# Kernel optimization log

Measured on AMD Instinct MI355X. Metric: run time of the kernel, lower is better.

The kernel has to match this reference:

```python
import jax, jax.numpy as jnp
import numpy as np

N_NODES = 50000
N_EDGES = 800000
D_FEAT = 128
HIDDEN = 128
OUT = 64
HEADS = 4


def setup_inputs() -> dict:
    key = jax.random.key(0)
    ks = jax.random.split(key, 12)
    s_in = 1.0 / np.sqrt(D_FEAT)
    s_h = 1.0 / np.sqrt(HIDDEN)
    x = jax.random.normal(ks[0], (N_NODES, D_FEAT), dtype=jnp.float32)
    edge_index = jax.random.randint(ks[1], (2, N_EDGES), 0, N_NODES, dtype=jnp.int32)
    return {
        "x": x,
        "edge_index": edge_index,
        # SAGEConv params: lin_l (aggregated neighbors), lin_r (root), bias
        "W_l": jax.random.normal(ks[2], (D_FEAT, HIDDEN), dtype=jnp.float32) * s_in,
        "W_r": jax.random.normal(ks[3], (D_FEAT, HIDDEN), dtype=jnp.float32) * s_in,
        "b_sage": jnp.zeros((HIDDEN,), dtype=jnp.float32),
        # GATConv params: lin_src, lin_dst (heads*hidden each), att vectors, bias
        "W_src": jax.random.normal(ks[4], (HIDDEN, HEADS * HIDDEN), dtype=jnp.float32) * s_h,
        "W_dst": jax.random.normal(ks[5], (HIDDEN, HEADS * HIDDEN), dtype=jnp.float32) * s_h,
        "att_src": jax.random.normal(ks[6], (HEADS, HIDDEN), dtype=jnp.float32) * s_h,
        "att_dst": jax.random.normal(ks[7], (HEADS, HIDDEN), dtype=jnp.float32) * s_h,
        "b_gat": jnp.zeros((HIDDEN,), dtype=jnp.float32),
        # Final Linear
        "W_lin": jax.random.normal(ks[8], (HIDDEN, OUT), dtype=jnp.float32) * s_h,
        "b_lin": jnp.zeros((OUT,), dtype=jnp.float32),
    }


def reference(x, edge_index, W_l, W_r, b_sage, W_src, W_dst, att_src, att_dst, b_gat, W_lin, b_lin):
    N = x.shape[0]
    src = edge_index[0]
    dst = edge_index[1]

    # ---- SAGEConv (mean aggregation): out = lin_l(mean_j x_j) + lin_r(x_i) + b ----
    agg = jax.ops.segment_sum(x[src], dst, num_segments=N)          # [N, d]
    cnt = jax.ops.segment_sum(jnp.ones_like(dst, dtype=x.dtype), dst, num_segments=N)
    mean_nbr = agg / jnp.maximum(cnt, 1.0)[:, None]
    h = mean_nbr @ W_l + x @ W_r + b_sage                           # [N, H*... no: [N, hidden]
    h = jax.nn.relu(h)

    # ---- GATConv (heads=4, concat=False -> mean over heads) ----
    H, C = att_src.shape
    hs = (h @ W_src).reshape(N, H, C)                               # source-transformed [N, H, C]
    hd = (h @ W_dst).reshape(N, H, C)                               # dest-transformed   [N, H, C]
    a_s = jnp.einsum('nhc,hc->nh', hs, att_src)                     # [N, H]
    a_d = jnp.einsum('nhc,hc->nh', hd, att_dst)                     # [N, H]
    e = jax.nn.leaky_relu(a_s[src] + a_d[dst], negative_slope=0.2)  # [E, H]
    # edge softmax over incoming edges per destination node
    e_max = jax.ops.segment_max(e, dst, num_segments=N)             # [N, H]
    e_exp = jnp.exp(e - e_max[dst])                                 # [E, H]
    denom = jax.ops.segment_sum(e_exp, dst, num_segments=N)         # [N, H]
    alpha = e_exp / denom[dst]                                      # [E, H]
    msg = hs[src] * alpha[:, :, None]                               # [E, H, C]
    out = jax.ops.segment_sum(msg, dst, num_segments=N)             # [N, H, C]
    out = out.mean(axis=1) + b_gat                                  # concat=False: avg heads
    out = jax.nn.relu(out)

    # ---- final Linear ----
    return out @ W_lin + b_lin
```

## Files before the change

### kernel.cpp

```cpp
#include <hip/hip_runtime.h>

#define D 128
#define HEADS 4

typedef __attribute__((ext_vector_type(8))) short short8;
typedef __attribute__((ext_vector_type(4))) float f32x4;

static __device__ __forceinline__ float leaky(float v) { return v > 0.f ? v : 0.2f * v; }

static __device__ __forceinline__ float2 bf2_to_f2(unsigned int u) {
    float2 r;
    union { unsigned int i; float f; } a, b;
    a.i = (u & 0xffffu) << 16;
    b.i = u & 0xffff0000u;
    r.x = a.f; r.y = b.f;
    return r;
}
static __device__ __forceinline__ float bf_to_f(unsigned short s) {
    union { unsigned int i; float f; } a;
    a.i = ((unsigned int)s) << 16;
    return a.f;
}
static __device__ __forceinline__ unsigned short f2bf(float f) {
    union { float f; unsigned int i; } v; v.f = f;
    unsigned int u = v.i;
    unsigned int r = (u + 0x7fffu + ((u >> 16) & 1u)) >> 16;
    return (unsigned short)r;
}

#define CPAD 16
#define PREP_CNT 107520
#define MAXBUCK 2048
#define BSLOT 1024
#define CH 8192

__global__ __launch_bounds__(256) void k_early(const float* __restrict__ x, int npairs,
                                               const float* __restrict__ Wl, const float* __restrict__ Wr,
                                               const float* __restrict__ Wsrc, const float* __restrict__ Wlin,
                                               const float* __restrict__ Wdst,
                                               const float* __restrict__ atts, const float* __restrict__ attd,
                                               unsigned short* __restrict__ Bh,
                                               unsigned short* __restrict__ Bg,
                                               unsigned short* __restrict__ Bf,
                                               float* __restrict__ wsd,
                                               unsigned int* __restrict__ xb) {
    int i = blockIdx.x * 256 + threadIdx.x;
    if (i < 32768) {
        int idx = i;
        int j = idx & 7, n16 = (idx >> 3) & 15, quad = (idx >> 7) & 3, rest = idx >> 9;
        int nc = rest & 7, kb = rest >> 3;
        int kk = kb * 32 + quad * 8 + j;
        int n = nc * 16 + n16;
        float v = (kk < 128) ? Wl[kk * 128 + n] : Wr[(kk - 128) * 128 + n];
        Bh[idx] = f2bf(v);
    } else if (i < 32768 + 65536) {
        int idx = i - 32768;
        int j = idx & 7, n16 = (idx >> 3) & 15, quad = (idx >> 7) & 3, rest = idx >> 9;
        int nc = rest & 7, kb = rest >> 3;
        int kk = kb * 32 + quad * 8 + j;
        int n = nc * 16 + n16;
        float v = Wsrc[(kk & 127) * 512 + (kk >> 7) * 128 + n];
        Bg[idx] = f2bf(v);
    } else if (i < 32768 + 65536 + 8192) {
        int idx = i - 98304;
        int j = idx & 7, n16 = (idx >> 3) & 15, quad = (idx >> 7) & 3, rest = idx >> 9;
        int nc = rest & 3, kb = rest >> 2;
        int kk = kb * 32 + quad * 8 + j;
        int n = nc * 16 + n16;
        Bf[idx] = f2bf(Wlin[kk * 64 + n]);
    } else if (i < PREP_CNT) {
        int tt = i - 106496;
        int k = tt >> 3, o = tt & 7;
        int hh = o & 3;
        const float* W = (o < 4) ? Wsrc : Wdst;
        const float* att = (o < 4) ? atts : attd;
        float acc = 0.f;
        for (int c = 0; c < 128; c++) acc += W[k * 512 + hh * 128 + c] * att[hh * 128 + c];
        wsd[k * 8 + o] = acc;
    } else {
        int p = i - PREP_CNT;
        if (p < npairs) {
            float2 v = *(const float2*)(x + (size_t)p * 2);
            xb[p] = (unsigned int)f2bf(v.x) | ((unsigned int)f2bf(v.y) << 16);
        }
    }
}

__global__ __launch_bounds__(256) void k_scatter1(const int* __restrict__ ei, int E, int nbuck,
                                                  int* __restrict__ bcur,
                                                  unsigned int* __restrict__ ebuf) {
    __shared__ unsigned int sval[CH];
    __shared__ unsigned short soff[CH];
    __shared__ int cnt[MAXBUCK];
    __shared__ int gbase[MAXBUCK];
    int t = threadIdx.x;
    int c0 = blockIdx.x * CH;
    int ecnt = E - c0; if (ecnt > CH) ecnt = CH;
    for (int i = t; i < MAXBUCK; i += 256) cnt[i] = 0;
    __syncthreads();
    for (int i = t; i < ecnt; i += 256) {
        int s = ei[c0 + i], d = ei[E + c0 + i];
        int b = d >> 5;
        soff[i] = (unsigned short)atomicAdd(&cnt[b], 1);
        sval[i] = (unsigned int)s | ((unsigned int)(d & 31) << 16) | ((unsigned int)b << 21);
    }
    __syncthreads();
    for (int b = t; b < nbuck; b += 256)
        if (cnt[b]) gbase[b] = (b << 10) + atomicAdd(&bcur[b * CPAD], cnt[b]);
    __syncthreads();
    for (int i = t; i < ecnt; i += 256) {
        unsigned int v = sval[i];
        int b = v >> 21;
        int pos = gbase[b] + soff[i];
        if (pos < ((b + 1) << 10)) ebuf[pos] = v & 0x1fffffu;
    }
}

#define BCAP 1024
__global__ __launch_bounds__(256) void k_build_sage(const unsigned int* __restrict__ ebuf,
                                                    const int* __restrict__ bcur,
                                                    const unsigned int* __restrict__ xb,
                                                    int* __restrict__ csr,
                                                    int* __restrict__ rowptr,
                                                    int* __restrict__ rowend,
                                                    unsigned int* __restrict__ meanb, int N) {
    __shared__ int cnt[32];
    __shared__ int excl[33];
    __shared__ unsigned char off[BCAP];
    __shared__ unsigned int rawv[BCAP];
    __shared__ int sorted[BCAP];
    int b = blockIdx.x, t = threadIdx.x;
    int e0 = b << 10;
    int ecnt = bcur[b * CPAD];
    if (ecnt > BCAP) ecnt = BCAP;
    if (t < 32) cnt[t] = 0;
    __syncthreads();
    for (int i = t; i < ecnt; i += 256) {
        unsigned int p = ebuf[e0 + i];
        rawv[i] = p;
        off[i] = (unsigned char)atomicAdd(&cnt[(p >> 16) & 31], 1);
    }
    __syncthreads();
    if (t == 0) {
        int run = 0;
        #pragma unroll
        for (int j = 0; j < 32; j++) { excl[j] = run; run += cnt[j]; }
        excl[32] = run;
    }
    __syncthreads();
    for (int i = t; i < ecnt; i += 256) {
        unsigned int p = rawv[i];
        int d = (p >> 16) & 31;
        sorted[excl[d] + off[i]] = (int)(p & 0xffffu);
    }
    __syncthreads();
    int nb0 = b << 5;
    if (t < 32 && nb0 + t < N) {
        rowptr[nb0 + t] = e0 + excl[t];
        rowend[nb0 + t] = e0 + excl[t + 1];
    }
    for (int i = t; i < ecnt; i += 256) csr[e0 + i] = sorted[i];
    int wv = t >> 6, lane = t & 63;
    for (int k = 0; k < 8; k++) {
        int local = wv * 8 + k;
        int node = nb0 + local;
        if (node >= N) continue;
        int le0 = excl[local], le1 = excl[local + 1];
        float ax = 0.f, ay = 0.f;
        int e = le0;
        for (; e + 3 < le1; e += 4) {
            int s0 = sorted[e], s1 = sorted[e + 1], s2 = sorted[e + 2], s3 = sorted[e + 3];
            unsigned int u0 = xb[(size_t)s0 * 64 + lane];
            unsigned int u1 = xb[(size_t)s1 * 64 + lane];
            unsigned int u2 = xb[(size_t)s2 * 64 + lane];
            unsigned int u3 = xb[(size_t)s3 * 64 + lane];
            float2 v0 = bf2_to_f2(u0), v1 = bf2_to_f2(u1), v2 = bf2_to_f2(u2), v3 = bf2_to_f2(u3);
            ax += (v0.x + v1.x) + (v2.x + v3.x);
            ay += (v0.y + v1.y) + (v2.y + v3.y);
        }
        for (; e < le1; e++) {
            float2 v0 = bf2_to_f2(xb[(size_t)sorted[e] * 64 + lane]);
            ax += v0.x; ay += v0.y;
        }
        int dg = le1 - le0;
        float inv = 1.0f / (float)(dg > 0 ? dg : 1);
        unsigned int o = (unsigned int)f2bf(ax * inv) | ((unsigned int)f2bf(ay * inv) << 16);
        __builtin_nontemporal_store(o, meanb + (size_t)node * 64 + lane);
    }
}

__global__ __launch_bounds__(256) void k_mfma_h(const unsigned short* __restrict__ A0,
                                                const unsigned short* __restrict__ A1,
                                                const unsigned short* __restrict__ Bp,
                                                const float* __restrict__ bias,
                                                const float* __restrict__ wsd,
                                                unsigned short* __restrict__ outb,
                                                float* __restrict__ a_s,
                                                float* __restrict__ a_d, int M) {
    const int NC = 8;
    __shared__ unsigned short sH[64][136];
    __shared__ float swsd[1024];
    int tid = threadIdx.x;
    int wave = tid >> 6;
    int lane = tid & 63;
    int row0 = blockIdx.x * 64 + wave * 16;
    int n16 = lane & 15, quad = lane >> 4;
    int arow = row0 + n16;
    int arowc = arow < M ? arow : 0;
    for (int i = tid; i < 1024; i += 256) swsd[i] = wsd[i];
    f32x4 acc[NC];
    #pragma unroll
    for (int i = 0; i < NC; i++) acc[i] = (f32x4){0.f, 0.f, 0.f, 0.f};
    #pragma unroll
    for (int kb = 0; kb < 8; kb++) {
        const unsigned short* ap = (kb < 4)
            ? (A0 + (size_t)arowc * 128 + kb * 32 + quad * 8)
            : (A1 + (size_t)arowc * 128 + (kb - 4) * 32 + quad * 8);
        short8 af = *(const short8*)ap;
        #pragma unroll
        for (int nc = 0; nc < NC; nc++) {
            short8 bf = *(const short8*)(Bp + ((((size_t)(kb * NC + nc) * 4 + quad) * 16 + n16) << 3));
            acc[nc] = __builtin_amdgcn_mfma_f32_16x16x32_bf16(af, bf, acc[nc], 0, 0, 0);
        }
    }
    int orow = row0 + quad * 4;
    int lrow = wave * 16 + quad * 4;
    #pragma unroll
    for (int r = 0; r < 4; r++) {
        int m = orow + r;
        #pragma unroll
        for (int nc = 0; nc < NC; nc++) {
            int col = nc * 16 + n16;
            float v = fmaxf(acc[nc][r] + bias[col], 0.f);
            unsigned short bv = f2bf(v);
            sH[lrow + r][col] = bv;
            if (m < M) outb[(size_t)m * 128 + col] = bv;
        }
    }
    __syncthreads();
    #pragma unroll
    for (int j = tid; j < 512; j += 256) {
        int m = j >> 3, o = j & 7;
        float accd = 0.f;
        #pragma unroll 4
        for (int k = 0; k < 128; k++)
            accd += bf_to_f(sH[m][k]) * swsd[k * 8 + o];
        int n = blockIdx.x * 64 + m;
        if (n < M) {
            if (o < 4) a_s[n * 4 + o] = accd;
            else       a_d[n * 4 + (o - 4)] = accd;
        }
    }
}

#define EDGE_CAP 192
__global__ __launch_bounds__(256) void k_gat_agg(const int* __restrict__ rowptr,
                                                 const int* __restrict__ rowend,
                                                 const int* __restrict__ csr,
                                                 const unsigned int* __restrict__ hb,
                                                 const float* __restrict__ a_s,
                                                 const float* __restrict__ a_d,
                                                 unsigned int* __restrict__ aggb, int N) {
    __shared__ int   sOff[4][EDGE_CAP];
    __shared__ float sAl[4][EDGE_CAP * 4];
    int wv = threadIdx.x >> 6;
    int lane = threadIdx.x & 63;
    int n = blockIdx.x * 4 + wv;
    bool active = n < N;
    int e0 = 0, deg = 0;
    float4 ad = {0.f, 0.f, 0.f, 0.f};
    if (active) {
        e0 = rowptr[n];
        deg = rowend[n] - e0;
        ad = *(const float4*)(a_d + (size_t)n * 4);
    }
    f32x4 psum = {0.f, 0.f, 0.f, 0.f};
    for (int base = 0; base < deg; base += 64) {
        int i = base + lane;
        if (i < deg) {
            int s = csr[e0 + i];
            float4 as = *(const float4*)(a_s + (size_t)s * 4);
            f32x4 w;
            w.x = __expf(leaky(as.x + ad.x));
            w.y = __expf(leaky(as.y + ad.y));
            w.z = __expf(leaky(as.z + ad.z));
            w.w = __expf(leaky(as.w + ad.w));
            psum += w;
            if (i < EDGE_CAP) {
                sOff[wv][i] = s << 8;
                *(f32x4*)&sAl[wv][i * 4] = w;
            }
        }
    }
    #pragma unroll
    for (int o = 32; o; o >>= 1) {
        psum.x += __shfl_xor(psum.x, o);
        psum.y += __shfl_xor(psum.y, o);
        psum.z += __shfl_xor(psum.z, o);
        psum.w += __shfl_xor(psum.w, o);
    }
    f32x4 inv;
    inv.x = psum.x > 0.f ? 0.25f / psum.x : 0.f;
    inv.y = psum.y > 0.f ? 0.25f / psum.y : 0.f;
    inv.z = psum.z > 0.f ? 0.25f / psum.z : 0.f;
    inv.w = psum.w > 0.f ? 0.25f / psum.w : 0.f;
    int capdeg = deg < EDGE_CAP ? deg : EDGE_CAP;
    for (int base = 0; base < capdeg; base += 64) {
        int i = base + lane;
        if (i < capdeg) {
            f32x4 w = *(f32x4*)&sAl[wv][i * 4];
            w *= inv;
            *(f32x4*)&sAl[wv][i * 4] = w;
        }
    }
    const char* hbL = (const char*)hb + lane * 4;
    float2 ac0 = {0, 0}, ac1 = {0, 0}, ac2 = {0, 0}, ac3 = {0, 0};
    int e = 0;
    for (; e + 7 < capdeg; e += 8) {
        unsigned int u[8];
        #pragma unroll
        for (int q = 0; q < 8; q++)
            u[q] = *(const unsigned int*)(hbL + sOff[wv][e + q]);
        #pragma unroll
        for (int q = 0; q < 8; q++) {
            f32x4 w = *(const f32x4*)&sAl[wv][(e + q) * 4];
            float2 v = bf2_to_f2(u[q]);
            ac0.x += w.x * v.x; ac0.y += w.x * v.y;
            ac1.x += w.y * v.x; ac1.y += w.y * v.y;
            ac2.x += w.z * v.x; ac2.y += w.z * v.y;
            ac3.x += w.w * v.x; ac3.y += w.w * v.y;
        }
    }
    for (; e + 3 < capdeg; e += 4) {
        unsigned int u[4];
        #pragma unroll
        for (int q = 0; q < 4; q++)
            u[q] = *(const unsigned int*)(hbL + sOff[wv][e + q]);
        #pragma unroll
        for (int q = 0; q < 4; q++) {
            f32x4 w = *(const f32x4*)&sAl[wv][(e + q) * 4];
            float2 v = bf2_to_f2(u[q]);
            ac0.x += w.x * v.x; ac0.y += w.x * v.y;
            ac1.x += w.y * v.x; ac1.y += w.y * v.y;
            ac2.x += w.z * v.x; ac2.y += w.z * v.y;
            ac3.x += w.w * v.x; ac3.y += w.w * v.y;
        }
    }
    for (; e < capdeg; e++) {
        unsigned int u0 = *(const unsigned int*)(hbL + sOff[wv][e]);
        f32x4 w0 = *(const f32x4*)&sAl[wv][e * 4];
        float2 v0 = bf2_to_f2(u0);
        ac0.x += w0.x * v0.x; ac0.y += w0.x * v0.y;
        ac1.x += w0.y * v0.x; ac1.y += w0.y * v0.y;
        ac2.x += w0.z * v0.x; ac2.y += w0.z * v0.y;
        ac3.x += w0.w * v0.x; ac3.y += w0.w * v0.y;
    }
    for (int i = EDGE_CAP; i < deg; i++) {
        int s = csr[e0 + i];
        float4 as = *(const float4*)(a_s + (size_t)s * 4);
        f32x4 w;
        w.x = __expf(leaky(as.x + ad.x)) * inv.x;
        w.y = __expf(leaky(as.y + ad.y)) * inv.y;
        w.z = __expf(leaky(as.z + ad.z)) * inv.z;
        w.w = __expf(leaky(as.w + ad.w)) * inv.w;
        float2 v0 = bf2_to_f2(hb[(size_t)s * 64 + lane]);
        ac0.x += w.x * v0.x; ac0.y += w.x * v0.y;
        ac1.x += w.y * v0.x; ac1.y += w.y * v0.y;
        ac2.x += w.z * v0.x; ac2.y += w.z * v0.y;
        ac3.x += w.w * v0.x; ac3.y += w.w * v0.y;
    }
    if (!active) return;
    unsigned int* rowu = aggb + (size_t)n * 256 + lane;
    unsigned int o0 = (unsigned int)f2bf(ac0.x) | ((unsigned int)f2bf(ac0.y) << 16);
    unsigned int o1 = (unsigned int)f2bf(ac1.x) | ((unsigned int)f2bf(ac1.y) << 16);
    unsigned int o2 = (unsigned int)f2bf(ac2.x) | ((unsigned int)f2bf(ac2.y) << 16);
    unsigned int o3 = (unsigned int)f2bf(ac3.x) | ((unsigned int)f2bf(ac3.y) << 16);
    __builtin_nontemporal_store(o0, rowu + 0);
    __builtin_nontemporal_store(o1, rowu + 64);
    __builtin_nontemporal_store(o2, rowu + 128);
    __builtin_nontemporal_store(o3, rowu + 192);
}

__global__ __launch_bounds__(256) void k_mfma_tail(const unsigned short* __restrict__ aggb,
                                                   const unsigned short* __restrict__ Bg,
                                                   const float* __restrict__ bg,
                                                   const unsigned short* __restrict__ Bf,
                                                   const float* __restrict__ bl,
                                                   float* __restrict__ out, int M) {
    __shared__ unsigned short sG[64][136];
    int wave = threadIdx.x >> 6;
    int lane = threadIdx.x & 63;
    int row0 = blockIdx.x * 64 + wave * 16;
    int n16 = lane & 15, quad = lane >> 4;
    {
        int arow = row0 + n16;
        int arowc = arow < M ? arow : 0;
        const unsigned short* ap = aggb + (size_t)arowc * 512 + quad * 8;
        f32x4 acc[8];
        #pragma unroll
        for (int i = 0; i < 8; i++) acc[i] = (f32x4){0.f, 0.f, 0.f, 0.f};
        #pragma unroll
        for (int kb = 0; kb < 16; kb++) {
            short8 af = *(const short8*)(ap + kb * 32);
            #pragma unroll
            for (int nc = 0; nc < 8; nc++) {
                short8 bf = *(const short8*)(Bg + ((((size_t)(kb * 8 + nc) * 4 + quad) * 16 + n16) << 3));
                acc[nc] = __builtin_amdgcn_mfma_f32_16x16x32_bf16(af, bf, acc[nc], 0, 0, 0);
            }
        }
        int lrow = wave * 16 + quad * 4;
        #pragma unroll
        for (int r = 0; r < 4; r++) {
            #pragma unroll
            for (int nc = 0; nc < 8; nc++) {
                int col = nc * 16 + n16;
                sG[lrow + r][col] = f2bf(fmaxf(acc[nc][r] + bg[col], 0.f));
            }
        }
    }
    __syncthreads();
    {
        f32x4 acc[4];
        #pragma unroll
        for (int i = 0; i < 4; i++) acc[i] = (f32x4){0.f, 0.f, 0.f, 0.f};
        #pragma unroll
        for (int kb = 0; kb < 4; kb++) {
            short8 af = *(const short8*)&sG[wave * 16 + n16][kb * 32 + quad * 8];
            #pragma unroll
            for (int nc = 0; nc < 4; nc++) {
                short8 bf = *(const short8*)(Bf + ((((size_t)(kb * 4 + nc) * 4 + quad) * 16 + n16) << 3));
                acc[nc] = __builtin_amdgcn_mfma_f32_16x16x32_bf16(af, bf, acc[nc], 0, 0, 0);
            }
        }
        int orow = row0 + quad * 4;
        #pragma unroll
        for (int r = 0; r < 4; r++) {
            int m = orow + r;
            if (m < M) {
                #pragma unroll
                for (int nc = 0; nc < 4; nc++) {
                    int col = nc * 16 + n16;
                    out[(size_t)m * 64 + col] = acc[nc][r] + bl[col];
                }
            }
        }
    }
}

extern "C" void kernel_launch(void* const* d_in, const int* in_sizes, int n_in,
                              void* d_out, int out_size, void* d_ws, size_t ws_size,
                              hipStream_t stream) {
    const float* x    = (const float*)d_in[0];
    const int*   ei   = (const int*)d_in[1];
    const float* Wl   = (const float*)d_in[2];
    const float* Wr   = (const float*)d_in[3];
    const float* bs   = (const float*)d_in[4];
    const float* Wsrc = (const float*)d_in[5];
    const float* Wdst = (const float*)d_in[6];
    const float* atts = (const float*)d_in[7];
    const float* attd = (const float*)d_in[8];
    const float* bg   = (const float*)d_in[9];
    const float* Wlin = (const float*)d_in[10];
    const float* bl   = (const float*)d_in[11];
    int N = in_sizes[0] / D;
    int E = in_sizes[1] / 2;
    int nbuck = (N + 31) >> 5;
    int npairs = N * 64;

    char* w = (char*)d_ws;
    auto alloc = [&](size_t bytes) {
        char* p = w;
        w += (bytes + 255) & ~(size_t)255;
        return p;
    };
    unsigned int* xb     = (unsigned int*)alloc((size_t)N * 256);
    unsigned int* meanb  = (unsigned int*)alloc((size_t)N * 256);
    unsigned int* hb     = (unsigned int*)alloc((size_t)N * 256);
    unsigned int* aggb   = (unsigned int*)alloc((size_t)N * 1024);
    unsigned short* Bh   = (unsigned short*)alloc(65536 * 2);
    unsigned short* Bg   = (unsigned short*)alloc(65536 * 2);
    unsigned short* Bf   = (unsigned short*)alloc(8192 * 2);
    float* a_s           = (float*)alloc((size_t)N * 16);
    float* a_d           = (float*)alloc((size_t)N * 16);
    float* wsd           = (float*)alloc(1024 * 4);
    int* rowptr          = (int*)alloc((size_t)N * 4);
    int* rowend          = (int*)alloc((size_t)N * 4);
    int* bcur            = (int*)alloc((size_t)MAXBUCK * CPAD * 4);
    unsigned int* ebuf   = (unsigned int*)alloc((size_t)MAXBUCK * BSLOT * 4);
    int* csr             = (int*)alloc((size_t)MAXBUCK * BSLOT * 4);
    (void)ws_size; (void)n_in; (void)out_size;

    hipMemsetAsync(bcur, 0, (size_t)MAXBUCK * CPAD * 4, stream);

    int workBlocks = (PREP_CNT + npairs + 255) / 256;
    k_early<<<workBlocks, 256, 0, stream>>>(x, npairs, Wl, Wr, Wsrc, Wlin, Wdst, atts, attd,
                                            Bh, Bg, Bf, wsd, xb);
    k_scatter1<<<(E + CH - 1) / CH, 256, 0, stream>>>(ei, E, nbuck, bcur, ebuf);
    k_build_sage<<<nbuck, 256, 0, stream>>>(ebuf, bcur, xb, csr, rowptr, rowend, meanb, N);

    k_mfma_h<<<(N + 63) / 64, 256, 0, stream>>>((const unsigned short*)meanb,
                                                (const unsigned short*)xb, Bh, bs, wsd,
                                                (unsigned short*)hb, a_s, a_d, N);
    k_gat_agg<<<(N + 3) / 4, 256, 0, stream>>>(rowptr, rowend, csr, hb, a_s, a_d, aggb, N);
    k_mfma_tail<<<(N + 63) / 64, 256, 0, stream>>>((const unsigned short*)aggb, Bg, bg,
                                                   Bf, bl, (float*)d_out, N);
}
```

Measured before the change: 260.0 us.

## Fuse edge scatter into prep kernel and simplify GAT aggregation loop

Merges the bucket scatter kernel into the early prep kernel by dispatching the first blocks to scatter work, removing one launch. The GAT aggregation inner loop now stores source indices instead of byte offsets, uses a single 4-way unrolled loop with tree-summed FMAs, and adds a block barrier. The fused kernel allocates the scatter's large shared-memory arrays for every block, which may reduce occupancy of the elementwise prep blocks, and the smaller unroll lowers memory-level parallelism in the gather.

```diff
diff --git a/kernel.cpp b/kernel.cpp
--- a/kernel.cpp
+++ b/kernel.cpp
@@ -35,6 +35,9 @@
 #define CH 8192
 
 __global__ __launch_bounds__(256) void k_early(const float* __restrict__ x, int npairs,
+                                               const int* __restrict__ ei, int E, int nbuck, int scatB,
+                                               int* __restrict__ bcur,
+                                               unsigned int* __restrict__ ebuf,
                                                const float* __restrict__ Wl, const float* __restrict__ Wr,
                                                const float* __restrict__ Wsrc, const float* __restrict__ Wlin,
                                                const float* __restrict__ Wdst,
@@ -44,7 +47,35 @@
                                                unsigned short* __restrict__ Bf,
                                                float* __restrict__ wsd,
                                                unsigned int* __restrict__ xb) {
-    int i = blockIdx.x * 256 + threadIdx.x;
+    __shared__ unsigned int sval[CH];
+    __shared__ unsigned short soff[CH];
+    __shared__ int cnt[MAXBUCK];
+    __shared__ int gbase[MAXBUCK];
+    int gb = blockIdx.x, t = threadIdx.x;
+    if (gb < scatB) {
+        int c0 = gb * CH;
+        int ecnt = E - c0; if (ecnt > CH) ecnt = CH;
+        for (int i = t; i < MAXBUCK; i += 256) cnt[i] = 0;
+        __syncthreads();
+        for (int i = t; i < ecnt; i += 256) {
+            int s = ei[c0 + i], d = ei[E + c0 + i];
+            int b = d >> 5;
+            soff[i] = (unsigned short)atomicAdd(&cnt[b], 1);
+            sval[i] = (unsigned int)s | ((unsigned int)(d & 31) << 16) | ((unsigned int)b << 21);
+        }
+        __syncthreads();
+        for (int b = t; b < nbuck; b += 256)
+            if (cnt[b]) gbase[b] = (b << 10) + atomicAdd(&bcur[b * CPAD], cnt[b]);
+        __syncthreads();
+        for (int i = t; i < ecnt; i += 256) {
+            unsigned int v = sval[i];
+            int b = v >> 21;
+            int pos = gbase[b] + soff[i];
+            if (pos < ((b + 1) << 10)) ebuf[pos] = v & 0x1fffffu;
+        }
+        return;
+    }
+    int i = (gb - scatB) * 256 + t;
     if (i < 32768) {
         int idx = i;
         int j = idx & 7, n16 = (idx >> 3) & 15, quad = (idx >> 7) & 3, rest = idx >> 9;
@@ -86,36 +117,6 @@
     }
 }
 
-__global__ __launch_bounds__(256) void k_scatter1(const int* __restrict__ ei, int E, int nbuck,
-                                                  int* __restrict__ bcur,
-                                                  unsigned int* __restrict__ ebuf) {
-    __shared__ unsigned int sval[CH];
-    __shared__ unsigned short soff[CH];
-    __shared__ int cnt[MAXBUCK];
-    __shared__ int gbase[MAXBUCK];
-    int t = threadIdx.x;
-    int c0 = blockIdx.x * CH;
-    int ecnt = E - c0; if (ecnt > CH) ecnt = CH;
-    for (int i = t; i < MAXBUCK; i += 256) cnt[i] = 0;
-    __syncthreads();
-    for (int i = t; i < ecnt; i += 256) {
-        int s = ei[c0 + i], d = ei[E + c0 + i];
-        int b = d >> 5;
-        soff[i] = (unsigned short)atomicAdd(&cnt[b], 1);
-        sval[i] = (unsigned int)s | ((unsigned int)(d & 31) << 16) | ((unsigned int)b << 21);
-    }
-    __syncthreads();
-    for (int b = t; b < nbuck; b += 256)
-        if (cnt[b]) gbase[b] = (b << 10) + atomicAdd(&bcur[b * CPAD], cnt[b]);
-    __syncthreads();
-    for (int i = t; i < ecnt; i += 256) {
-        unsigned int v = sval[i];
-        int b = v >> 21;
-        int pos = gbase[b] + soff[i];
-        if (pos < ((b + 1) << 10)) ebuf[pos] = v & 0x1fffffu;
-    }
-}
-
 #define BCAP 1024
 __global__ __launch_bounds__(256) void k_build_sage(const unsigned int* __restrict__ ebuf,
                                                     const int* __restrict__ bcur,
@@ -261,7 +262,7 @@
                                                  const float* __restrict__ a_s,
                                                  const float* __restrict__ a_d,
                                                  unsigned int* __restrict__ aggb, int N) {
-    __shared__ int   sOff[4][EDGE_CAP];
+    __shared__ int   sSrc[4][EDGE_CAP];
     __shared__ float sAl[4][EDGE_CAP * 4];
     int wv = threadIdx.x >> 6;
     int lane = threadIdx.x & 63;
@@ -287,7 +288,7 @@
             w.w = __expf(leaky(as.w + ad.w));
             psum += w;
             if (i < EDGE_CAP) {
-                sOff[wv][i] = s << 8;
+                sSrc[wv][i] = s;
                 *(f32x4*)&sAl[wv][i * 4] = w;
             }
         }
@@ -313,42 +314,33 @@
             *(f32x4*)&sAl[wv][i * 4] = w;
         }
     }
-    const char* hbL = (const char*)hb + lane * 4;
+    __syncthreads();
     float2 ac0 = {0, 0}, ac1 = {0, 0}, ac2 = {0, 0}, ac3 = {0, 0};
     int e = 0;
-    for (; e + 7 < capdeg; e += 8) {
-        unsigned int u[8];
-        #pragma unroll
-        for (int q = 0; q < 8; q++)
-            u[q] = *(const unsigned int*)(hbL + sOff[wv][e + q]);
-        #pragma unroll
-        for (int q = 0; q < 8; q++) {
-            f32x4 w = *(const f32x4*)&sAl[wv][(e + q) * 4];
-            float2 v = bf2_to_f2(u[q]);
-            ac0.x += w.x * v.x; ac0.y += w.x * v.y;
-            ac1.x += w.y * v.x; ac1.y += w.y * v.y;
-            ac2.x += w.z * v.x; ac2.y += w.z * v.y;
-            ac3.x += w.w * v.x; ac3.y += w.w * v.y;
-        }
-    }
     for (; e + 3 < capdeg; e += 4) {
-        unsigned int u[4];
-        #pragma unroll
-        for (int q = 0; q < 4; q++)
-            u[q] = *(const unsigned int*)(hbL + sOff[wv][e + q]);
-        #pragma unroll
-        for (int q = 0; q < 4; q++) {
-            f32x4 w = *(const f32x4*)&sAl[wv][(e + q) * 4];
-            float2 v = bf2_to_f2(u[q]);
-            ac0.x += w.x * v.x; ac0.y += w.x * v.y;
-            ac1.x += w.y * v.x; ac1.y += w.y * v.y;
-            ac2.x += w.z * v.x; ac2.y += w.z * v.y;
-            ac3.x += w.w * v.x; ac3.y += w.w * v.y;
-        }
+        int s0 = sSrc[wv][e], s1 = sSrc[wv][e + 1], s2 = sSrc[wv][e + 2], s3 = sSrc[wv][e + 3];
+        f32x4 w0 = *(const f32x4*)&sAl[wv][e * 4];
+        f32x4 w1 = *(const f32x4*)&sAl[wv][e * 4 + 4];
+        f32x4 w2 = *(const f32x4*)&sAl[wv][e * 4 + 8];
+        f32x4 w3 = *(const f32x4*)&sAl[wv][e * 4 + 12];
+        unsigned int u0 = hb[(size_t)s0 * 64 + lane];
+        unsigned int u1 = hb[(size_t)s1 * 64 + lane];
+        unsigned int u2 = hb[(size_t)s2 * 64 + lane];
+        unsigned int u3 = hb[(size_t)s3 * 64 + lane];
+        float2 v0 = bf2_to_f2(u0), v1 = bf2_to_f2(u1), v2 = bf2_to_f2(u2), v3 = bf2_to_f2(u3);
+        ac0.x += w0.x * v0.x + w1.x * v1.x + w2.x * v2.x + w3.x * v3.x;
+        ac0.y += w0.x * v0.y + w1.x * v1.y + w2.x * v2.y + w3.x * v3.y;
+        ac1.x += w0.y * v0.x + w1.y * v1.x + w2.y * v2.x + w3.y * v3.x;
+        ac1.y += w0.y * v0.y + w1.y * v1.y + w2.y * v2.y + w3.y * v3.y;
+        ac2.x += w0.z * v0.x + w1.z * v1.x + w2.z * v2.x + w3.z * v3.x;
+        ac2.y += w0.z * v0.y + w1.z * v1.y + w2.z * v2.y + w3.z * v3.y;
+        ac3.x += w0.w * v0.x + w1.w * v1.x + w2.w * v2.x + w3.w * v3.x;
+        ac3.y += w0.w * v0.y + w1.w * v1.y + w2.w * v2.y + w3.w * v3.y;
     }
     for (; e < capdeg; e++) {
-        unsigned int u0 = *(const unsigned int*)(hbL + sOff[wv][e]);
+        int s0 = sSrc[wv][e];
         f32x4 w0 = *(const f32x4*)&sAl[wv][e * 4];
+        unsigned int u0 = hb[(size_t)s0 * 64 + lane];
         float2 v0 = bf2_to_f2(u0);
         ac0.x += w0.x * v0.x; ac0.y += w0.x * v0.y;
         ac1.x += w0.y * v0.x; ac1.y += w0.y * v0.y;
@@ -492,10 +484,12 @@
 
     hipMemsetAsync(bcur, 0, (size_t)MAXBUCK * CPAD * 4, stream);
 
+    int scatB = (E + CH - 1) / CH;
     int workBlocks = (PREP_CNT + npairs + 255) / 256;
-    k_early<<<workBlocks, 256, 0, stream>>>(x, npairs, Wl, Wr, Wsrc, Wlin, Wdst, atts, attd,
-                                            Bh, Bg, Bf, wsd, xb);
-    k_scatter1<<<(E + CH - 1) / CH, 256, 0, stream>>>(ei, E, nbuck, bcur, ebuf);
+    k_early<<<scatB + workBlocks, 256, 0, stream>>>(x, npairs, ei, E, nbuck, scatB,
+                                                    bcur, ebuf,
+                                                    Wl, Wr, Wsrc, Wlin, Wdst, atts, attd,
+                                                    Bh, Bg, Bf, wsd, xb);
     k_build_sage<<<nbuck, 256, 0, stream>>>(ebuf, bcur, xb, csr, rowptr, rowend, meanb, N);
 
     k_mfma_h<<<(N + 63) / 64, 256, 0, stream>>>((const unsigned short*)meanb,
```

Measured after the change: 247.1 us. -4.9%, faster.
